# Kernel tuning notes

Measured on AMD Instinct MI355X. Metric: run time of the kernel, lower is better.

## Reference

```python
import jax, jax.numpy as jnp
import numpy as np

N = 50000
NEG_SLOPE = 0.2


def _gat_layer(x, src, dst, W, a_src, a_dst, b, heads, out_ch, concat):
    # x: [N, F_in]; W: [F_in, heads*out_ch]; a_src/a_dst: [heads, out_ch]; b: bias
    h = (x @ W).reshape(N, heads, out_ch)                      # [N,H,C]
    s_src = jnp.einsum('nhc,hc->nh', h, a_src)                 # [N,H]
    s_dst = jnp.einsum('nhc,hc->nh', h, a_dst)                 # [N,H]
    e = jax.nn.leaky_relu(s_src[src] + s_dst[dst], NEG_SLOPE)  # [E,H]
    # segment softmax over edges sharing the same destination node
    m = jax.ops.segment_max(e, dst, num_segments=N)
    m = jax.lax.stop_gradient(jnp.where(jnp.isfinite(m), m, 0.0))
    w = jnp.exp(e - m[dst])
    denom = jax.ops.segment_sum(w, dst, num_segments=N)
    alpha = w / (denom[dst] + 1e-16)                           # [E,H]
    out = jax.ops.segment_sum(alpha[:, :, None] * h[src], dst, num_segments=N)  # [N,H,C]
    out = out.reshape(N, heads * out_ch) if concat else out.mean(axis=1)
    return out + b


def setup_inputs() -> dict:
    key = jax.random.key(0)
    ks = jax.random.split(key, 16)
    F_in, Hd, H1, H3, F_out = 128, 64, 4, 6, 64
    E = 800000
    x = jax.random.normal(ks[0], (N, F_in), dtype=jnp.float32)
    edge_index = jax.random.randint(ks[1], (2, E), 0, N, dtype=jnp.int64)

    def glorot(k, shape, fan_in):
        return jax.random.normal(k, shape, dtype=jnp.float32) * (1.0 / np.sqrt(fan_in))

    params = {
        'W1': glorot(ks[2], (F_in, H1 * Hd), F_in),
        'a1_src': glorot(ks[3], (H1, Hd), Hd),
        'a1_dst': glorot(ks[4], (H1, Hd), Hd),
        'b1': jnp.zeros((H1 * Hd,), dtype=jnp.float32),
        'W2': glorot(ks[5], (H1 * Hd, H1 * Hd), H1 * Hd),
        'a2_src': glorot(ks[6], (H1, Hd), Hd),
        'a2_dst': glorot(ks[7], (H1, Hd), Hd),
        'b2': jnp.zeros((H1 * Hd,), dtype=jnp.float32),
        'W3': glorot(ks[8], (H1 * Hd, H3 * F_out), H1 * Hd),
        'a3_src': glorot(ks[9], (H3, F_out), F_out),
        'a3_dst': glorot(ks[10], (H3, F_out), F_out),
        'b3': jnp.zeros((F_out,), dtype=jnp.float32),
    }
    return {'x': x, 'edge_index': edge_index, **params}


def reference(x, edge_index, W1, a1_src, a1_dst, b1, W2, a2_src, a2_dst, b2, W3, a3_src, a3_dst, b3):
    # PyG GATConv default add_self_loops=True
    loops = jnp.arange(N, dtype=edge_index.dtype)
    src = jnp.concatenate([edge_index[0], loops])
    dst = jnp.concatenate([edge_index[1], loops])
    x1 = jax.nn.elu(_gat_layer(x, src, dst, W1, a1_src, a1_dst, b1, heads=4, out_ch=64, concat=True))
    x2 = jax.nn.elu(_gat_layer(x1, src, dst, W2, a2_src, a2_dst, b2, heads=4, out_ch=64, concat=True))
    x3 = _gat_layer(x2, src, dst, W3, a3_src, a3_dst, b3, heads=6, out_ch=64, concat=False)
    return x3
```

## Files before the change

### kernel.cpp

```cpp
#include <hip/hip_runtime.h>
#include <hip/hip_bf16.h>
#include <hip/hip_fp16.h>
#include <math.h>

#define NNODES 50000

typedef __attribute__((ext_vector_type(8))) short short8v;
typedef __attribute__((ext_vector_type(4))) float f32x4;
typedef unsigned short ushort_t;
typedef unsigned int uint_t;

__device__ inline ushort_t f2bf_bits(float v) {
    union { __hip_bfloat16 b; ushort_t u; } c;
    c.b = __float2bfloat16(v);
    return c.u;
}
__device__ inline float bfbits2f(ushort_t u) {
    union { __hip_bfloat16 b; ushort_t u; } c;
    c.u = u;
    return __bfloat162float(c.b);
}
__device__ inline ushort_t f2h_bits(float v) {
    union { __half h; ushort_t u; } c;
    c.h = __float2half(v);
    return c.u;
}
__device__ inline void cvt2(uint_t u, float& a, float& b) {
    union { uint_t u; __half2 h; } c; c.u = u;
    a = __low2float(c.h); b = __high2float(c.h);
}

__global__ __launch_bounds__(256)
void split_kernel(const float4* __restrict__ in, ushort4* __restrict__ hi,
                  ushort4* __restrict__ lo, int n4) {
    int i = blockIdx.x * blockDim.x + threadIdx.x;
    if (i >= n4) return;
    float4 v = in[i];
    ushort4 h, l;
    h.x = f2bf_bits(v.x); l.x = f2bf_bits(v.x - bfbits2f(h.x));
    h.y = f2bf_bits(v.y); l.y = f2bf_bits(v.y - bfbits2f(h.y));
    h.z = f2bf_bits(v.z); l.z = f2bf_bits(v.z - bfbits2f(h.z));
    h.w = f2bf_bits(v.w); l.w = f2bf_bits(v.w - bfbits2f(h.w));
    hi[i] = h; lo[i] = l;
}

__global__ __launch_bounds__(256)
void wprep_kernel(const float* __restrict__ W, ushort_t* __restrict__ hiT,
                  ushort_t* __restrict__ loT, int K, int N) {
    int idx = blockIdx.x * blockDim.x + threadIdx.x;
    if (idx >= K * N) return;
    int k = idx / N, n = idx - k * N;
    float v = W[idx];
    ushort_t hb = f2bf_bits(v);
    hiT[(size_t)n * K + k] = hb;
    loT[(size_t)n * K + k] = f2bf_bits(v - bfbits2f(hb));
}

template<int H>
__global__ __launch_bounds__(256)
void gemm_fused(const ushort_t* __restrict__ Ahi, const ushort_t* __restrict__ Alo,
                const ushort_t* __restrict__ Bhi, const ushort_t* __restrict__ Blo,
                ushort_t* __restrict__ h16, float* __restrict__ ssrc,
                float* __restrict__ sdst, const float* __restrict__ a_src,
                const float* __restrict__ a_dst, int M, int K) {
    __shared__ char smem[32768];
    __shared__ float sSs[128][2], sDs[128][2];

    const int tid = threadIdx.x;
    const int lane = tid & 63;
    const int wid = tid >> 6;
    const int wm = wid >> 1, wn = wid & 1;
    const int bm = blockIdx.y * 128;
    const int bn = blockIdx.x * 128;
    const int r15 = lane & 15;
    const int g4 = lane >> 4;

    if (tid < 128) { sSs[tid][0] = 0.f; sSs[tid][1] = 0.f;
                     sDs[tid][0] = 0.f; sDs[tid][1] = 0.f; }

    char* As_hi = smem;
    char* As_lo = smem + 8192;
    char* Bs_hi = smem + 16384;
    char* Bs_lo = smem + 24576;

    const int srow = tid >> 1;
    const int sch  = (tid & 1) * 2;
    const size_t arow = (size_t)(bm + srow) * K;
    const size_t brow = (size_t)(bn + srow) * K;

    f32x4 acc[4][4] = {};

    for (int k0 = 0; k0 < K; k0 += 32) {
        short8v a0 = *(const short8v*)&Ahi[arow + k0 + sch * 8];
        short8v a1 = *(const short8v*)&Ahi[arow + k0 + sch * 8 + 8];
        short8v l0 = *(const short8v*)&Alo[arow + k0 + sch * 8];
        short8v l1 = *(const short8v*)&Alo[arow + k0 + sch * 8 + 8];
        short8v b0 = *(const short8v*)&Bhi[brow + k0 + sch * 8];
        short8v b1 = *(const short8v*)&Bhi[brow + k0 + sch * 8 + 8];
        short8v m0 = *(const short8v*)&Blo[brow + k0 + sch * 8];
        short8v m1 = *(const short8v*)&Blo[brow + k0 + sch * 8 + 8];
        __syncthreads();
        *(short8v*)(As_hi + sch * 2048 + srow * 16)       = a0;
        *(short8v*)(As_hi + (sch + 1) * 2048 + srow * 16) = a1;
        *(short8v*)(As_lo + sch * 2048 + srow * 16)       = l0;
        *(short8v*)(As_lo + (sch + 1) * 2048 + srow * 16) = l1;
        *(short8v*)(Bs_hi + sch * 2048 + srow * 16)       = b0;
        *(short8v*)(Bs_hi + (sch + 1) * 2048 + srow * 16) = b1;
        *(short8v*)(Bs_lo + sch * 2048 + srow * 16)       = m0;
        *(short8v*)(Bs_lo + (sch + 1) * 2048 + srow * 16) = m1;
        __syncthreads();

        short8v ah[4], al[4], bh[4], bl[4];
        #pragma unroll
        for (int mi = 0; mi < 4; ++mi) {
            int row = wm * 64 + mi * 16 + r15;
            ah[mi] = *(const short8v*)(As_hi + g4 * 2048 + row * 16);
            al[mi] = *(const short8v*)(As_lo + g4 * 2048 + row * 16);
        }
        #pragma unroll
        for (int nj = 0; nj < 4; ++nj) {
            int row = wn * 64 + nj * 16 + r15;
            bh[nj] = *(const short8v*)(Bs_hi + g4 * 2048 + row * 16);
            bl[nj] = *(const short8v*)(Bs_lo + g4 * 2048 + row * 16);
        }
        #pragma unroll
        for (int mi = 0; mi < 4; ++mi)
            #pragma unroll
            for (int nj = 0; nj < 4; ++nj) {
                acc[mi][nj] = __builtin_amdgcn_mfma_f32_16x16x32_bf16(ah[mi], bh[nj], acc[mi][nj], 0, 0, 0);
                acc[mi][nj] = __builtin_amdgcn_mfma_f32_16x16x32_bf16(ah[mi], bl[nj], acc[mi][nj], 0, 0, 0);
                acc[mi][nj] = __builtin_amdgcn_mfma_f32_16x16x32_bf16(al[mi], bh[nj], acc[mi][nj], 0, 0, 0);
            }
    }
    __syncthreads();

    ushort_t* h2 = (ushort_t*)smem;
    const int headg = (bn >> 6) + wn;
    float asv[4], adv[4];
    #pragma unroll
    for (int nj = 0; nj < 4; ++nj) {
        asv[nj] = a_src[headg * 64 + nj * 16 + r15];
        adv[nj] = a_dst[headg * 64 + nj * 16 + r15];
    }
    #pragma unroll
    for (int mi = 0; mi < 4; ++mi) {
        #pragma unroll
        for (int reg = 0; reg < 4; ++reg) {
            int row_l = wm * 64 + mi * 16 + g4 * 4 + reg;
            int csw = ((row_l >> 2) & 3) << 2;
            float pS = 0.f, pD = 0.f;
            #pragma unroll
            for (int nj = 0; nj < 4; ++nj) {
                float v = acc[mi][nj][reg];
                int col_l = wn * 64 + nj * 16 + r15;
                h2[row_l * 128 + (col_l ^ csw)] = f2h_bits(v);
                pS += v * asv[nj];
                pD += v * adv[nj];
            }
            #pragma unroll
            for (int off = 1; off < 16; off <<= 1) {
                pS += __shfl_xor(pS, off);
                pD += __shfl_xor(pD, off);
            }
            if (r15 == 0 && bm + row_l < M) {
                atomicAdd(&sSs[row_l][wn], pS);
                atomicAdd(&sDs[row_l][wn], pD);
            }
        }
    }
    __syncthreads();

    uint_t* plane = (uint_t*)h16 + (size_t)(bn >> 7) * ((size_t)NNODES * 64);
    for (int u = tid; u < 128 * 64; u += 256) {
        int n_l = u >> 6, c = u & 63;
        if (bm + n_l < M) {
            int csw = ((n_l >> 2) & 3) << 2;
            uint_t lo = h2[n_l * 128 + (c ^ csw)];
            uint_t hi = h2[n_l * 128 + 64 + (c ^ csw)];
            plane[(size_t)(bm + n_l) * 64 + c] = lo | (hi << 16);
        }
    }
    {
        int row = tid >> 1, hl = tid & 1;
        if (bm + row < M) {
            int hg = (bn >> 6) + hl;
            ssrc[(size_t)(bm + row) * H + hg] = sSs[row][hl];
            sdst[(size_t)(bm + row) * H + hg] = sDs[row][hl];
        }
    }
}

__global__ void deg_kernel(const int* __restrict__ ei, int E, int Nn,
                           int* __restrict__ deg) {
    int e = blockIdx.x * blockDim.x + threadIdx.x;
    int tot = E + Nn;
    if (e >= tot) return;
    int d = (e < E) ? ei[E + e] : (e - E);
    atomicAdd(&deg[d], 1);
}

__global__ __launch_bounds__(1024)
void scan_kernel(const int* __restrict__ deg, int* __restrict__ offs, int n) {
    __shared__ int sh[1024];
    __shared__ int carry_sh;
    int t = threadIdx.x;
    if (t == 0) carry_sh = 0;
    __syncthreads();
    for (int base = 0; base < n; base += 1024) {
        int i = base + t;
        int v = (i < n) ? deg[i] : 0;
        sh[t] = v;
        __syncthreads();
        for (int off = 1; off < 1024; off <<= 1) {
            int add = (t >= off) ? sh[t - off] : 0;
            __syncthreads();
            sh[t] += add;
            __syncthreads();
        }
        int carry = carry_sh;
        if (i < n) offs[i + 1] = carry + sh[t];
        __syncthreads();
        if (t == 1023) carry_sh = carry + sh[1023];
        __syncthreads();
    }
    if (t == 0) offs[0] = 0;
}

__global__ void copy_int_kernel(const int* __restrict__ src, int* __restrict__ dst, int n) {
    int i = blockIdx.x * blockDim.x + threadIdx.x;
    if (i < n) dst[i] = src[i];
}

__global__ void scatter_kernel(const int* __restrict__ ei, int E, int Nn,
                               int* __restrict__ cursor, int* __restrict__ csr_src) {
    int e = blockIdx.x * blockDim.x + threadIdx.x;
    int tot = E + Nn;
    if (e >= tot) return;
    int s, d;
    if (e < E) { s = ei[e]; d = ei[E + e]; }
    else       { s = d = e - E; }
    int pos = atomicAdd(&cursor[d], 1);
    csr_src[pos] = s;
}

template<int H>
__device__ inline void loadS(const float* __restrict__ p, float* v) {
    if constexpr (H == 4) {
        float4 t = *(const float4*)p;
        v[0] = t.x; v[1] = t.y; v[2] = t.z; v[3] = t.w;
    } else {
        const float2* q = (const float2*)p;
        float2 a = q[0], b = q[1], c = q[2];
        v[0] = a.x; v[1] = a.y; v[2] = b.x; v[3] = b.y; v[4] = c.x; v[5] = c.y;
    }
}

template<int H>
__global__ __launch_bounds__(256)
void smw_kernel(const float* __restrict__ ssrc, const float* __restrict__ sdst,
                const int* __restrict__ offs, const int* __restrict__ csr,
                float* __restrict__ wbuf, float* __restrict__ rden, int Nn) {
    int wid = (blockIdx.x * blockDim.x + threadIdx.x) >> 6;
    int lane = threadIdx.x & 63;
    if (wid >= Nn) return;
    int beg = offs[wid], end = offs[wid + 1];
    float sd[H], mx[H], den[H];
    #pragma unroll
    for (int h = 0; h < H; ++h) {
        sd[h] = sdst[wid * H + h];
        mx[h] = -INFINITY;
        den[h] = 0.f;
    }
    for (int i = beg + lane; i < end; i += 64) {
        int s = csr[i];
        float sv[H];
        loadS<H>(ssrc + (size_t)s * H, sv);
        #pragma unroll
        for (int h = 0; h < H; ++h) mx[h] = fmaxf(mx[h], sv[h]);
    }
    #pragma unroll
    for (int h = 0; h < H; ++h) {
        #pragma unroll
        for (int off = 32; off; off >>= 1) mx[h] = fmaxf(mx[h], __shfl_xor(mx[h], off));
        float t = mx[h] + sd[h];
        mx[h] = t > 0.f ? t : 0.2f * t;
    }
    for (int i = beg + lane; i < end; i += 64) {
        int s = csr[i];
        float sv[H];
        loadS<H>(ssrc + (size_t)s * H, sv);
        #pragma unroll
        for (int h = 0; h < H; ++h) {
            float sc = sv[h] + sd[h];
            sc = sc > 0.f ? sc : 0.2f * sc;
            float w = __expf(sc - mx[h]);
            wbuf[(size_t)i * H + h] = w;
            den[h] += w;
        }
    }
    #pragma unroll
    for (int h = 0; h < H; ++h) {
        #pragma unroll
        for (int off = 32; off; off >>= 1) den[h] += __shfl_xor(den[h], off);
    }
    if (lane == 0) {
        #pragma unroll
        for (int h = 0; h < H; ++h) rden[wid * H + h] = 1.f / (den[h] + 1e-16f);
    }
}

template<int H, bool MEAN>
__global__ __launch_bounds__(256)
void agg_kernel(const ushort_t* __restrict__ h16, const float* __restrict__ wbuf,
                const float* __restrict__ rden, const int* __restrict__ offs,
                const int* __restrict__ csr, const float* __restrict__ bias,
                float* __restrict__ outf, ushort_t* __restrict__ ohi,
                ushort_t* __restrict__ olo, int Nn) {
    constexpr int P = H / 2;
    int wid = (blockIdx.x * blockDim.x + threadIdx.x) >> 6;
    int lane = threadIdx.x & 63;
    if (wid >= Nn) return;
    int beg = offs[wid], end = offs[wid + 1];
    const uint_t* up = (const uint_t*)h16;
    const size_t psz = (size_t)Nn * 64;

    constexpr int U = (H == 4) ? 8 : 4;
    float acc0[H] = {}, acc1[H] = {};
    int i = beg;
    for (; i + U <= end; i += U) {
        int s[U];
        #pragma unroll
        for (int j = 0; j < U; ++j) s[j] = csr[i + j];
        uint_t g[U][P];
        #pragma unroll
        for (int j = 0; j < U; ++j)
            #pragma unroll
            for (int p = 0; p < P; ++p)
                g[j][p] = up[(size_t)p * psz + (size_t)s[j] * 64 + lane];
        float w[U][H];
        #pragma unroll
        for (int j = 0; j < U; ++j) {
            if constexpr (H == 4) {
                float4 t = *(const float4*)&wbuf[(size_t)(i + j) * 4];
                w[j][0] = t.x; w[j][1] = t.y; w[j][2] = t.z; w[j][3] = t.w;
            } else {
                const float2* q = (const float2*)&wbuf[(size_t)(i + j) * 6];
                float2 a = q[0], b = q[1], c = q[2];
                w[j][0] = a.x; w[j][1] = a.y; w[j][2] = b.x;
                w[j][3] = b.y; w[j][4] = c.x; w[j][5] = c.y;
            }
        }
        #pragma unroll
        for (int j = 0; j < U; ++j) {
            float v[H];
            #pragma unroll
            for (int p = 0; p < P; ++p) cvt2(g[j][p], v[2 * p], v[2 * p + 1]);
            float* a = (j & 1) ? acc1 : acc0;
            #pragma unroll
            for (int h = 0; h < H; ++h) a[h] += w[j][h] * v[h];
        }
    }
    for (; i < end; ++i) {
        int s = csr[i];
        float v[H];
        #pragma unroll
        for (int p = 0; p < P; ++p) {
            uint_t g = up[(size_t)p * psz + (size_t)s * 64 + lane];
            cvt2(g, v[2 * p], v[2 * p + 1]);
        }
        #pragma unroll
        for (int h = 0; h < H; ++h) acc0[h] += wbuf[(size_t)i * H + h] * v[h];
    }

    if (!MEAN) {
        #pragma unroll
        for (int h = 0; h < H; ++h) {
            float val = (acc0[h] + acc1[h]) * rden[wid * H + h] + bias[h * 64 + lane];
            val = val > 0.f ? val : expm1f(val);
            size_t idx = (size_t)wid * (H * 64) + h * 64 + lane;
            ushort_t hb = f2bf_bits(val);
            ohi[idx] = hb;
            olo[idx] = f2bf_bits(val - bfbits2f(hb));
        }
    } else {
        float m = 0.f;
        #pragma unroll
        for (int h = 0; h < H; ++h) m += (acc0[h] + acc1[h]) * rden[wid * H + h];
        outf[(size_t)wid * 64 + lane] = m * (1.f / (float)H) + bias[lane];
    }
}

extern "C" void kernel_launch(void* const* d_in, const int* in_sizes, int n_in,
                              void* d_out, int out_size, void* d_ws, size_t ws_size,
                              hipStream_t stream) {
    const float* x     = (const float*)d_in[0];
    const int*   ei    = (const int*)d_in[1];
    const float* W1    = (const float*)d_in[2];
    const float* a1s   = (const float*)d_in[3];
    const float* a1d   = (const float*)d_in[4];
    const float* b1    = (const float*)d_in[5];
    const float* W2    = (const float*)d_in[6];
    const float* a2s   = (const float*)d_in[7];
    const float* a2d   = (const float*)d_in[8];
    const float* b2    = (const float*)d_in[9];
    const float* W3    = (const float*)d_in[10];
    const float* a3s   = (const float*)d_in[11];
    const float* a3d   = (const float*)d_in[12];
    const float* b3    = (const float*)d_in[13];
    float* out = (float*)d_out;

    const int Nn = NNODES;
    const int E  = in_sizes[1] / 2;
    const int Etot = E + Nn;

    char* p = (char*)d_ws;
    auto carve = [&](size_t bytes) {
        char* r = p;
        p += (bytes + 255) & ~(size_t)255;
        return (void*)r;
    };
    ushort_t* h16   = (ushort_t*)carve((size_t)Nn * 384 * 2);
    ushort_t* R1    = (ushort_t*)carve((size_t)Nn * 256 * 4);
    ushort_t* x_hi  = R1;
    ushort_t* x_lo  = R1 + (size_t)Nn * 128;
    ushort_t* x1_hi = R1;
    ushort_t* x1_lo = R1 + (size_t)Nn * 256;
    ushort_t* w1hi  = (ushort_t*)carve((size_t)128 * 256 * 2);
    ushort_t* w1lo  = (ushort_t*)carve((size_t)128 * 256 * 2);
    ushort_t* w2hi  = (ushort_t*)carve((size_t)256 * 256 * 2);
    ushort_t* w2lo  = (ushort_t*)carve((size_t)256 * 256 * 2);
    ushort_t* w3hi  = (ushort_t*)carve((size_t)256 * 384 * 2);
    ushort_t* w3lo  = (ushort_t*)carve((size_t)256 * 384 * 2);
    float* ssrc   = (float*)carve((size_t)Nn * 6 * 4);
    float* sdst   = (float*)carve((size_t)Nn * 6 * 4);
    float* rden   = (float*)carve((size_t)Nn * 6 * 4);
    float* wbuf   = (float*)carve((size_t)Etot * 6 * 4);
    int*   deg    = (int*)carve((size_t)Nn * 4);
    int*   offs   = (int*)carve((size_t)(Nn + 1) * 4);
    int*   cursor = (int*)carve((size_t)Nn * 4);
    int*   csr    = (int*)carve((size_t)Etot * 4);

    hipMemsetAsync(deg, 0, (size_t)Nn * 4, stream);
    {
        int nb = (Etot + 255) / 256;
        deg_kernel<<<nb, 256, 0, stream>>>(ei, E, Nn, deg);
        scan_kernel<<<1, 1024, 0, stream>>>(deg, offs, Nn);
        copy_int_kernel<<<(Nn + 255) / 256, 256, 0, stream>>>(offs, cursor, Nn);
        scatter_kernel<<<nb, 256, 0, stream>>>(ei, E, Nn, cursor, csr);
    }

    {
        int n4 = Nn * 128 / 4;
        split_kernel<<<(n4 + 255) / 256, 256, 0, stream>>>(
            (const float4*)x, (ushort4*)x_hi, (ushort4*)x_lo, n4);
        wprep_kernel<<<(128 * 256 + 255) / 256, 256, 0, stream>>>(W1, w1hi, w1lo, 128, 256);
        wprep_kernel<<<(256 * 256 + 255) / 256, 256, 0, stream>>>(W2, w2hi, w2lo, 256, 256);
        wprep_kernel<<<(256 * 384 + 255) / 256, 256, 0, stream>>>(W3, w3hi, w3lo, 256, 384);
    }

    const int node_blocks = (Nn + 3) / 4;
    const int gemm_rows = (Nn + 127) / 128;

    {
        dim3 g(2, gemm_rows);
        gemm_fused<4><<<g, 256, 0, stream>>>(x_hi, x_lo, w1hi, w1lo, h16,
                                             ssrc, sdst, a1s, a1d, Nn, 128);
        smw_kernel<4><<<node_blocks, 256, 0, stream>>>(ssrc, sdst, offs, csr, wbuf, rden, Nn);
        agg_kernel<4, false><<<node_blocks, 256, 0, stream>>>(h16, wbuf, rden, offs, csr, b1,
                                                              nullptr, x1_hi, x1_lo, Nn);
    }
    {
        dim3 g(2, gemm_rows);
        gemm_fused<4><<<g, 256, 0, stream>>>(x1_hi, x1_lo, w2hi, w2lo, h16,
                                             ssrc, sdst, a2s, a2d, Nn, 256);
        smw_kernel<4><<<node_blocks, 256, 0, stream>>>(ssrc, sdst, offs, csr, wbuf, rden, Nn);
        agg_kernel<4, false><<<node_blocks, 256, 0, stream>>>(h16, wbuf, rden, offs, csr, b2,
                                                              nullptr, x1_hi, x1_lo, Nn);
    }
    {
        dim3 g(3, gemm_rows);
        gemm_fused<6><<<g, 256, 0, stream>>>(x1_hi, x1_lo, w3hi, w3lo, h16,
                                             ssrc, sdst, a3s, a3d, Nn, 256);
        smw_kernel<6><<<node_blocks, 256, 0, stream>>>(ssrc, sdst, offs, csr, wbuf, rden, Nn);
        agg_kernel<6, true><<<node_blocks, 256, 0, stream>>>(h16, wbuf, rden, offs, csr, b3,
                                                             out, nullptr, nullptr, Nn);
    }
}
```

Measured before the change: 676.5 us.

## Use global per-head max for softmax shift, parallelize CSR scan, merge weight prep

```diff
diff --git a/kernel.cpp b/kernel.cpp
--- a/kernel.cpp
+++ b/kernel.cpp
@@ -28,6 +28,13 @@
 __device__ inline void cvt2(uint_t u, float& a, float& b) {
     union { uint_t u; __half2 h; } c; c.u = u;
     a = __low2float(c.h); b = __high2float(c.h);
+}
+__device__ inline uint_t fmap(float f) {
+    uint_t b = __float_as_uint(f);
+    return (b & 0x80000000u) ? ~b : (b | 0x80000000u);
+}
+__device__ inline float funmap(uint_t u) {
+    return __uint_as_float((u & 0x80000000u) ? (u & 0x7FFFFFFFu) : ~u);
 }
 
 __global__ __launch_bounds__(256)
@@ -45,15 +52,26 @@
 }
 
 __global__ __launch_bounds__(256)
-void wprep_kernel(const float* __restrict__ W, ushort_t* __restrict__ hiT,
-                  ushort_t* __restrict__ loT, int K, int N) {
+void wprep_all(const float* __restrict__ W1, const float* __restrict__ W2,
+               const float* __restrict__ W3,
+               ushort_t* __restrict__ w1h, ushort_t* __restrict__ w1l,
+               ushort_t* __restrict__ w2h, ushort_t* __restrict__ w2l,
+               ushort_t* __restrict__ w3h, ushort_t* __restrict__ w3l) {
     int idx = blockIdx.x * blockDim.x + threadIdx.x;
-    if (idx >= K * N) return;
+    const float* W; ushort_t* hT; ushort_t* lT; int K, N;
+    if (idx < 128 * 256) { W = W1; hT = w1h; lT = w1l; K = 128; N = 256; }
+    else if (idx < 128 * 256 + 256 * 256) {
+        idx -= 128 * 256; W = W2; hT = w2h; lT = w2l; K = 256; N = 256;
+    } else {
+        idx -= 128 * 256 + 256 * 256;
+        if (idx >= 256 * 384) return;
+        W = W3; hT = w3h; lT = w3l; K = 256; N = 384;
+    }
     int k = idx / N, n = idx - k * N;
     float v = W[idx];
     ushort_t hb = f2bf_bits(v);
-    hiT[(size_t)n * K + k] = hb;
-    loT[(size_t)n * K + k] = f2bf_bits(v - bfbits2f(hb));
+    hT[(size_t)n * K + k] = hb;
+    lT[(size_t)n * K + k] = f2bf_bits(v - bfbits2f(hb));
 }
 
 template<int H>
@@ -61,10 +79,12 @@
 void gemm_fused(const ushort_t* __restrict__ Ahi, const ushort_t* __restrict__ Alo,
                 const ushort_t* __restrict__ Bhi, const ushort_t* __restrict__ Blo,
                 ushort_t* __restrict__ h16, float* __restrict__ ssrc,
-                float* __restrict__ sdst, const float* __restrict__ a_src,
-                const float* __restrict__ a_dst, int M, int K) {
+                float* __restrict__ sdst, uint_t* __restrict__ gmaxu,
+                const float* __restrict__ a_src, const float* __restrict__ a_dst,
+                int M, int K) {
     __shared__ char smem[32768];
     __shared__ float sSs[128][2], sDs[128][2];
+    __shared__ uint_t gblk[2];
 
     const int tid = threadIdx.x;
     const int lane = tid & 63;
@@ -77,6 +97,7 @@
 
     if (tid < 128) { sSs[tid][0] = 0.f; sSs[tid][1] = 0.f;
                      sDs[tid][0] = 0.f; sDs[tid][1] = 0.f; }
+    if (tid < 2) gblk[tid] = 0;
 
     char* As_hi = smem;
     char* As_lo = smem + 8192;
@@ -184,10 +205,14 @@
         int row = tid >> 1, hl = tid & 1;
         if (bm + row < M) {
             int hg = (bn >> 6) + hl;
-            ssrc[(size_t)(bm + row) * H + hg] = sSs[row][hl];
+            float vS = sSs[row][hl];
+            ssrc[(size_t)(bm + row) * H + hg] = vS;
             sdst[(size_t)(bm + row) * H + hg] = sDs[row][hl];
-        }
-    }
+            atomicMax(&gblk[hl], fmap(vS));
+        }
+    }
+    __syncthreads();
+    if (tid < 2) atomicMax(&gmaxu[(bn >> 6) + tid], gblk[tid]);
 }
 
 __global__ void deg_kernel(const int* __restrict__ ei, int E, int Nn,
@@ -200,35 +225,47 @@
 }
 
 __global__ __launch_bounds__(1024)
-void scan_kernel(const int* __restrict__ deg, int* __restrict__ offs, int n) {
+void scan1_kernel(const int* __restrict__ deg, int* __restrict__ offs,
+                  int* __restrict__ bsum, int n) {
     __shared__ int sh[1024];
-    __shared__ int carry_sh;
     int t = threadIdx.x;
-    if (t == 0) carry_sh = 0;
+    int i = blockIdx.x * 1024 + t;
+    int v = (i < n) ? deg[i] : 0;
+    sh[t] = v;
     __syncthreads();
-    for (int base = 0; base < n; base += 1024) {
-        int i = base + t;
-        int v = (i < n) ? deg[i] : 0;
-        sh[t] = v;
+    for (int off = 1; off < 1024; off <<= 1) {
+        int add = (t >= off) ? sh[t - off] : 0;
         __syncthreads();
-        for (int off = 1; off < 1024; off <<= 1) {
-            int add = (t >= off) ? sh[t - off] : 0;
-            __syncthreads();
-            sh[t] += add;
-            __syncthreads();
-        }
-        int carry = carry_sh;
-        if (i < n) offs[i + 1] = carry + sh[t];
+        sh[t] += add;
         __syncthreads();
-        if (t == 1023) carry_sh = carry + sh[1023];
-        __syncthreads();
-    }
-    if (t == 0) offs[0] = 0;
-}
-
-__global__ void copy_int_kernel(const int* __restrict__ src, int* __restrict__ dst, int n) {
+    }
+    if (i < n) offs[i + 1] = sh[t];
+    if (t == 1023) bsum[blockIdx.x] = sh[1023];
+}
+
+__global__ __launch_bounds__(64)
+void scan2_kernel(const int* __restrict__ bsum, int* __restrict__ bexcl, int nb) {
+    int t = threadIdx.x;
+    int v = (t < nb) ? bsum[t] : 0;
+    int orig = v;
+    #pragma unroll
+    for (int off = 1; off < 64; off <<= 1) {
+        int u = __shfl_up(v, off);
+        if (t >= off) v += u;
+    }
+    if (t < nb) bexcl[t] = v - orig;
+}
+
+__global__ void scan3_kernel(const int* __restrict__ deg, int* __restrict__ offs,
+                             const int* __restrict__ bexcl, int* __restrict__ cursor,
+                             int n) {
     int i = blockIdx.x * blockDim.x + threadIdx.x;
-    if (i < n) dst[i] = src[i];
+    if (i == 0) offs[0] = 0;
+    if (i < n) {
+        int inc = offs[i + 1] + bexcl[i >> 10];
+        offs[i + 1] = inc;
+        cursor[i] = inc - deg[i];
+    }
 }
 
 __global__ void scatter_kernel(const int* __restrict__ ei, int E, int Nn,
@@ -258,8 +295,9 @@
 template<int H>
 __global__ __launch_bounds__(256)
 void smw_kernel(const float* __restrict__ ssrc, const float* __restrict__ sdst,
-                const int* __restrict__ offs, const int* __restrict__ csr,
-                float* __restrict__ wbuf, float* __restrict__ rden, int Nn) {
+                const uint_t* __restrict__ gmaxu, const int* __restrict__ offs,
+                const int* __restrict__ csr, float* __restrict__ wbuf,
+                float* __restrict__ rden, int Nn) {
     int wid = (blockIdx.x * blockDim.x + threadIdx.x) >> 6;
     int lane = threadIdx.x & 63;
     if (wid >= Nn) return;
@@ -268,22 +306,9 @@
     #pragma unroll
     for (int h = 0; h < H; ++h) {
         sd[h] = sdst[wid * H + h];
-        mx[h] = -INFINITY;
+        float t = funmap(gmaxu[h]) + sd[h];
+        mx[h] = t > 0.f ? t : 0.2f * t;
         den[h] = 0.f;
-    }
-    for (int i = beg + lane; i < end; i += 64) {
-        int s = csr[i];
-        float sv[H];
-        loadS<H>(ssrc + (size_t)s * H, sv);
-        #pragma unroll
-        for (int h = 0; h < H; ++h) mx[h] = fmaxf(mx[h], sv[h]);
-    }
-    #pragma unroll
-    for (int h = 0; h < H; ++h) {
-        #pragma unroll
-        for (int off = 32; off; off >>= 1) mx[h] = fmaxf(mx[h], __shfl_xor(mx[h], off));
-        float t = mx[h] + sd[h];
-        mx[h] = t > 0.f ? t : 0.2f * t;
     }
     for (int i = beg + lane; i < end; i += 64) {
         int s = csr[i];
@@ -439,13 +464,19 @@
     int*   offs   = (int*)carve((size_t)(Nn + 1) * 4);
     int*   cursor = (int*)carve((size_t)Nn * 4);
     int*   csr    = (int*)carve((size_t)Etot * 4);
+    uint_t* gmaxu = (uint_t*)carve(18 * 4);
+    int*   bsum   = (int*)carve(64 * 4);
+    int*   bexcl  = (int*)carve(64 * 4);
 
     hipMemsetAsync(deg, 0, (size_t)Nn * 4, stream);
+    hipMemsetAsync(gmaxu, 0, 18 * 4, stream);
     {
         int nb = (Etot + 255) / 256;
+        int nsb = (Nn + 1023) / 1024;
         deg_kernel<<<nb, 256, 0, stream>>>(ei, E, Nn, deg);
-        scan_kernel<<<1, 1024, 0, stream>>>(deg, offs, Nn);
-        copy_int_kernel<<<(Nn + 255) / 256, 256, 0, stream>>>(offs, cursor, Nn);
+        scan1_kernel<<<nsb, 1024, 0, stream>>>(deg, offs, bsum, Nn);
+        scan2_kernel<<<1, 64, 0, stream>>>(bsum, bexcl, nsb);
+        scan3_kernel<<<(Nn + 255) / 256, 256, 0, stream>>>(deg, offs, bexcl, cursor, Nn);
         scatter_kernel<<<nb, 256, 0, stream>>>(ei, E, Nn, cursor, csr);
     }
 
@@ -453,9 +484,9 @@
         int n4 = Nn * 128 / 4;
         split_kernel<<<(n4 + 255) / 256, 256, 0, stream>>>(
             (const float4*)x, (ushort4*)x_hi, (ushort4*)x_lo, n4);
-        wprep_kernel<<<(128 * 256 + 255) / 256, 256, 0, stream>>>(W1, w1hi, w1lo, 128, 256);
-        wprep_kernel<<<(256 * 256 + 255) / 256, 256, 0, stream>>>(W2, w2hi, w2lo, 256, 256);
-        wprep_kernel<<<(256 * 384 + 255) / 256, 256, 0, stream>>>(W3, w3hi, w3lo, 256, 384);
+        int wtot = 128 * 256 + 256 * 256 + 256 * 384;
+        wprep_all<<<(wtot + 255) / 256, 256, 0, stream>>>(W1, W2, W3, w1hi, w1lo,
+                                                          w2hi, w2lo, w3hi, w3lo);
     }
 
     const int node_blocks = (Nn + 3) / 4;
@@ -464,24 +495,27 @@
     {
         dim3 g(2, gemm_rows);
         gemm_fused<4><<<g, 256, 0, stream>>>(x_hi, x_lo, w1hi, w1lo, h16,
-                                             ssrc, sdst, a1s, a1d, Nn, 128);
-        smw_kernel<4><<<node_blocks, 256, 0, stream>>>(ssrc, sdst, offs, csr, wbuf, rden, Nn);
+                                             ssrc, sdst, gmaxu + 0, a1s, a1d, Nn, 128);
+        smw_kernel<4><<<node_blocks, 256, 0, stream>>>(ssrc, sdst, gmaxu + 0, offs, csr,
+                                                       wbuf, rden, Nn);
         agg_kernel<4, false><<<node_blocks, 256, 0, stream>>>(h16, wbuf, rden, offs, csr, b1,
                                                               nullptr, x1_hi, x1_lo, Nn);
     }
     {
         dim3 g(2, gemm_rows);
         gemm_fused<4><<<g, 256, 0, stream>>>(x1_hi, x1_lo, w2hi, w2lo, h16,
-                                             ssrc, sdst, a2s, a2d, Nn, 256);
-        smw_kernel<4><<<node_blocks, 256, 0, stream>>>(ssrc, sdst, offs, csr, wbuf, rden, Nn);
+                                             ssrc, sdst, gmaxu + 6, a2s, a2d, Nn, 256);
+        smw_kernel<4><<<node_blocks, 256, 0, stream>>>(ssrc, sdst, gmaxu + 6, offs, csr,
+                                                       wbuf, rden, Nn);
         agg_kernel<4, false><<<node_blocks, 256, 0, stream>>>(h16, wbuf, rden, offs, csr, b2,
                                                               nullptr, x1_hi, x1_lo, Nn);
     }
     {
         dim3 g(3, gemm_rows);
         gemm_fused<6><<<g, 256, 0, stream>>>(x1_hi, x1_lo, w3hi, w3lo, h16,
-                                             ssrc, sdst, a3s, a3d, Nn, 256);
-        smw_kernel<6><<<node_blocks, 256, 0, stream>>>(ssrc, sdst, offs, csr, wbuf, rden, Nn);
+                                             ssrc, sdst, gmaxu + 12, a3s, a3d, Nn, 256);
+        smw_kernel<6><<<node_blocks, 256, 0, stream>>>(ssrc, sdst, gmaxu + 12, offs, csr,
+                                                       wbuf, rden, Nn);
         agg_kernel<6, true><<<node_blocks, 256, 0, stream>>>(h16, wbuf, rden, offs, csr, b3,
                                                              out, nullptr, nullptr, Nn);
     }
```

Result: faster. 573.2 us (-15.3%).
